# Optimization experiments

Hardware: AMD Instinct MI355X
Metric: run time of the kernel (lower is better)

Reference implementation:

```python
import jax, jax.numpy as jnp
import numpy as np

N, E, G = 100000, 1600000, 64   # nodes, edges, graphs
IN, H, OUT = 32, 128, 3


def setup_inputs() -> dict:
    key = jax.random.key(0)
    ks = jax.random.split(key, 24)
    def w(k, i, o):
        return (jax.random.normal(k, (i, o), jnp.float32) / np.sqrt(i)).astype(jnp.float32)
    inp = {
        "x": jax.random.normal(ks[0], (N, IN), jnp.float32),
        "edge_index": jax.random.randint(ks[1], (2, E), 0, N, dtype=jnp.int32).astype(jnp.int64),
        "batch": jnp.sort(jax.random.randint(ks[2], (N,), 0, G, dtype=jnp.int32)).astype(jnp.int64),
        # SAGEConv layer 0 (in->hidden): lin_l (neighbors, with bias), lin_r (root, no bias)
        "Wl0": w(ks[3], IN, H), "bl0": jnp.zeros((H,), jnp.float32), "Wr0": w(ks[4], IN, H),
        # SAGEConv layers 1,2 (hidden->hidden)
        "Wl1": w(ks[5], H, H), "bl1": jnp.zeros((H,), jnp.float32), "Wr1": w(ks[6], H, H),
        "Wl2": w(ks[7], H, H), "bl2": jnp.zeros((H,), jnp.float32), "Wr2": w(ks[8], H, H),
        # output head
        "Wfc": w(ks[9], H, OUT), "bfc": jnp.zeros((OUT,), jnp.float32),
        # aux MLP on (dim1, dim3)
        "Wa1": w(ks[10], 2, H), "ba1": jnp.zeros((H,), jnp.float32),
        "Wa2": w(ks[11], H, H), "ba2": jnp.zeros((H,), jnp.float32),
        "Wao": w(ks[12], H, 1), "bao": jnp.zeros((1,), jnp.float32),
    }
    return inp


def _sage_conv(x, src, dst, Wl, bl, Wr):
    # PyG SAGEConv (mean aggr): out = lin_l(mean_{j in N(i)} x_j) + lin_r(x_i)
    msg = x[src]                                   # [E, d] gather
    agg = jax.ops.segment_sum(msg, dst, num_segments=N)
    cnt = jax.ops.segment_sum(jnp.ones((src.shape[0],), x.dtype), dst, num_segments=N)
    mean = agg / jnp.maximum(cnt, 1.0)[:, None]
    return mean @ Wl + bl + x @ Wr


def reference(x, edge_index, batch,
              Wl0, bl0, Wr0, Wl1, bl1, Wr1, Wl2, bl2, Wr2,
              Wfc, bfc, Wa1, ba1, Wa2, ba2, Wao, bao):
    src, dst = edge_index[0], edge_index[1]
    h = jax.nn.relu(_sage_conv(x, src, dst, Wl0, bl0, Wr0))   # dropout is identity in eval
    h = jax.nn.relu(_sage_conv(h, src, dst, Wl1, bl1, Wr1))
    h = jax.nn.relu(_sage_conv(h, src, dst, Wl2, bl2, Wr2))
    main = h @ Wfc + bfc                                      # [N, 3]
    dim1, dim3 = main[:, 0], main[:, 2]
    aux_in = jnp.stack([dim1, dim3], axis=-1)                 # [N, 2]
    a = jax.nn.relu(aux_in @ Wa1 + ba1)
    a = jax.nn.relu(a @ Wa2 + ba2)
    aux_out = (a @ Wao + bao)[:, 0]                           # [N]
    final = jnp.stack([dim1, aux_out, dim3], axis=-1)         # [N, 3]
    # global mean pool over graph ids
    s = jax.ops.segment_sum(final, batch, num_segments=G)
    c = jax.ops.segment_sum(jnp.ones((final.shape[0],), final.dtype), batch, num_segments=G)
    return s / jnp.maximum(c, 1.0)[:, None]                   # [G, 3]
```

## Files before the change

### kernel.cpp

```cpp
#include <hip/hip_runtime.h>

#define NR 128
#define PART_CH 4096
typedef unsigned short ushortT;
typedef __attribute__((ext_vector_type(8))) short short8;
typedef __attribute__((ext_vector_type(4))) float float4v;

__device__ __forceinline__ unsigned short f32_to_bf16_rne(float f) {
    unsigned u = __float_as_uint(f);
    unsigned r = (u + 0x7fffu + ((u >> 16) & 1u)) >> 16;
    return (unsigned short)r;
}

__device__ __forceinline__ void accum8(float* acc, uint4 v) {
    unsigned u[4] = {v.x, v.y, v.z, v.w};
#pragma unroll
    for (int q = 0; q < 4; q++) {
        acc[2 * q]     += __uint_as_float(u[q] << 16);
        acc[2 * q + 1] += __uint_as_float(u[q] & 0xffff0000u);
    }
}


__launch_bounds__(256)
__global__ void bucket_count(const int* __restrict__ dst, int* __restrict__ bcnt, int E, int NB) {
    __shared__ int h[1024];
    int t = threadIdx.x;
    for (int j = t; j < NB; j += 256) h[j] = 0;
    __syncthreads();
    int e0 = blockIdx.x * PART_CH;
    int e1 = min(e0 + PART_CH, E);
    for (int e = e0 + t; e < e1; e += 256) atomicAdd(&h[dst[e] >> 7], 1);
    __syncthreads();
    for (int j = t; j < NB; j += 256) {
        int v = h[j];
        if (v) atomicAdd(&bcnt[j], v);
    }
}

__launch_bounds__(256)
__global__ void bucket_scan(const int* __restrict__ bcnt, int* __restrict__ bstart,
                            int* __restrict__ gcur, int NB, int E) {
    __shared__ int sh[256];
    int t = threadIdx.x;
    int v[4];
    int tot = 0;
#pragma unroll
    for (int j = 0; j < 4; j++) {
        int idx = t * 4 + j;
        v[j] = (idx < NB) ? bcnt[idx] : 0;
        tot += v[j];
    }
    sh[t] = tot;
    __syncthreads();
    for (int off = 1; off < 256; off <<= 1) {
        int add = (t >= off) ? sh[t - off] : 0;
        __syncthreads();
        sh[t] += add;
        __syncthreads();
    }
    int run = sh[t] - tot;
#pragma unroll
    for (int j = 0; j < 4; j++) {
        int idx = t * 4 + j;
        if (idx < NB) { bstart[idx] = run; gcur[idx] = run; }
        run += v[j];
    }
    if (t == 0) bstart[NB] = E;
}

__launch_bounds__(256)
__global__ void partition_edges(const int* __restrict__ src, const int* __restrict__ dst,
                                int* __restrict__ gcur, unsigned* __restrict__ packed,
                                int E, int NB) {
    __shared__ int hist[1024];
    __shared__ int base[1024];
    int t = threadIdx.x;
    int e0 = blockIdx.x * PART_CH;
    int e1 = min(e0 + PART_CH, E);
    for (int j = t; j < NB; j += 256) hist[j] = 0;
    __syncthreads();
    for (int e = e0 + t; e < e1; e += 256) atomicAdd(&hist[dst[e] >> 7], 1);
    __syncthreads();
    for (int j = t; j < NB; j += 256) {
        int h = hist[j];
        base[j] = h ? atomicAdd(&gcur[j], h) : 0;
    }
    __syncthreads();
    for (int j = t; j < NB; j += 256) hist[j] = base[j];
    __syncthreads();
    for (int e = e0 + t; e < e1; e += 256) {
        int d = dst[e];
        int b = d >> 7;
        int pos = atomicAdd(&hist[b], 1);
        packed[pos] = (unsigned)src[e] | ((unsigned)(d & (NR - 1)) << 17);
    }
}

__launch_bounds__(256)
__global__ void bucket_sort(const unsigned* __restrict__ packed, const int* __restrict__ bstart,
                            int* __restrict__ row_start, int* __restrict__ srcs, int N) {
    __shared__ int cnt[NR];
    __shared__ int sc[NR];
    __shared__ int cur[NR];
    int b = blockIdx.x, t = threadIdx.x;
    int nb0 = b * NR;
    int nnode = min(NR, N - nb0);
    int lo = bstart[b], hi = bstart[b + 1];
    if (t < NR) cnt[t] = 0;
    __syncthreads();
    for (int j = lo + t; j < hi; j += 256) atomicAdd(&cnt[packed[j] >> 17], 1);
    __syncthreads();
    if (t < NR) sc[t] = cnt[t];
    __syncthreads();
    for (int off = 1; off < NR; off <<= 1) {
        int add = (t >= off && t < NR) ? sc[t - off] : 0;
        __syncthreads();
        if (t < NR) sc[t] += add;
        __syncthreads();
    }
    if (t < nnode) {
        int s = lo + sc[t] - cnt[t];
        row_start[nb0 + t] = s;
        cur[t] = s;
    }
    if (t == 0 && nb0 + nnode == N) row_start[N] = hi;
    __syncthreads();
    for (int j = lo + t; j < hi; j += 256) {
        unsigned pk = packed[j];
        int pos = atomicAdd(&cur[pk >> 17], 1);
        srcs[pos] = (int)(pk & 0x1FFFFu);
    }
}


__global__ void to_bf16_vec(const float* __restrict__ in, ushortT* __restrict__ out, int n4) {
    int t = blockIdx.x * 256 + threadIdx.x;
    if (t < n4) {
        float4 v = ((const float4*)in)[t];
        ushort4 o;
        o.x = f32_to_bf16_rne(v.x);
        o.y = f32_to_bf16_rne(v.y);
        o.z = f32_to_bf16_rne(v.z);
        o.w = f32_to_bf16_rne(v.w);
        ((ushort4*)out)[t] = o;
    }
}


__global__ void prep_wt(const float* __restrict__ Wl, const float* __restrict__ Wr,
                        ushortT* __restrict__ Wt, int KH) {
    int KT = 2 * KH;
    int tid = blockIdx.x * 256 + threadIdx.x;
    if (tid >= 128 * KT) return;
    int col = tid / KT, k = tid - col * KT;
    float v = (k < KH) ? Wl[k * 128 + col] : Wr[(k - KH) * 128 + col];
    int pos = (k + 8 * col) & (KT - 1);
    Wt[col * KT + pos] = f32_to_bf16_rne(v);
}

__global__ void prep_w1(const float* __restrict__ W, ushortT* __restrict__ Wt) {
    int tid = blockIdx.x * 256 + threadIdx.x;
    if (tid >= 128 * 128) return;
    int col = tid >> 7, k = tid & 127;
    int pos = (k + 8 * col) & 127;
    Wt[col * 128 + pos] = f32_to_bf16_rne(W[k * 128 + col]);
}


template <int CPN>
__launch_bounds__(256)
__global__ void aggregate_mean_bf16(const uint4* __restrict__ hin, ushortT* __restrict__ out,
                                    const int* __restrict__ srcs, const int* __restrict__ rs, int n) {
    constexpr int TPN = CPN / 2;
    int tid = blockIdx.x * 256 + threadIdx.x;
    if (tid >= n * TPN) return;
    int i = tid / TPN;
    int c = tid & (TPN - 1);
    int lo = rs[i], hi = rs[i + 1];
    float acc0[8], acc1[8];
#pragma unroll
    for (int q = 0; q < 8; q++) { acc0[q] = 0.f; acc1[q] = 0.f; }
    int e = lo;
    for (; e + 4 <= hi; e += 4) {
        int s0 = srcs[e], s1 = srcs[e + 1], s2 = srcs[e + 2], s3 = srcs[e + 3];
        uint4 a0 = hin[(size_t)s0 * CPN + c];
        uint4 b0 = hin[(size_t)s0 * CPN + c + TPN];
        uint4 a1 = hin[(size_t)s1 * CPN + c];
        uint4 b1 = hin[(size_t)s1 * CPN + c + TPN];
        uint4 a2 = hin[(size_t)s2 * CPN + c];
        uint4 b2 = hin[(size_t)s2 * CPN + c + TPN];
        uint4 a3 = hin[(size_t)s3 * CPN + c];
        uint4 b3 = hin[(size_t)s3 * CPN + c + TPN];
        accum8(acc0, a0); accum8(acc1, b0);
        accum8(acc0, a1); accum8(acc1, b1);
        accum8(acc0, a2); accum8(acc1, b2);
        accum8(acc0, a3); accum8(acc1, b3);
    }
    for (; e < hi; ++e) {
        int s = srcs[e];
        accum8(acc0, hin[(size_t)s * CPN + c]);
        accum8(acc1, hin[(size_t)s * CPN + c + TPN]);
    }
    float inv = 1.0f / (float)max(hi - lo, 1);
    uint4 o0, o1;
    o0.x = (unsigned)f32_to_bf16_rne(acc0[0] * inv) | ((unsigned)f32_to_bf16_rne(acc0[1] * inv) << 16);
    o0.y = (unsigned)f32_to_bf16_rne(acc0[2] * inv) | ((unsigned)f32_to_bf16_rne(acc0[3] * inv) << 16);
    o0.z = (unsigned)f32_to_bf16_rne(acc0[4] * inv) | ((unsigned)f32_to_bf16_rne(acc0[5] * inv) << 16);
    o0.w = (unsigned)f32_to_bf16_rne(acc0[6] * inv) | ((unsigned)f32_to_bf16_rne(acc0[7] * inv) << 16);
    o1.x = (unsigned)f32_to_bf16_rne(acc1[0] * inv) | ((unsigned)f32_to_bf16_rne(acc1[1] * inv) << 16);
    o1.y = (unsigned)f32_to_bf16_rne(acc1[2] * inv) | ((unsigned)f32_to_bf16_rne(acc1[3] * inv) << 16);
    o1.z = (unsigned)f32_to_bf16_rne(acc1[4] * inv) | ((unsigned)f32_to_bf16_rne(acc1[5] * inv) << 16);
    o1.w = (unsigned)f32_to_bf16_rne(acc1[6] * inv) | ((unsigned)f32_to_bf16_rne(acc1[7] * inv) << 16);
    ((uint4*)out)[(size_t)i * CPN + c] = o0;
    ((uint4*)out)[(size_t)i * CPN + c + TPN] = o1;
}


template <int KH, bool OUT_BF16>
__launch_bounds__(256, 2)
__global__ void gemm_mfma(const ushortT* __restrict__ Am, const ushortT* __restrict__ Ah,
                          const ushortT* __restrict__ Wt, const float* __restrict__ bias,
                          float* __restrict__ outf, ushortT* __restrict__ outbf, int n) {
    constexpr int KT = 2 * KH;
    __shared__ ushortT sW[128 * KT];
    int t = threadIdx.x;
    constexpr int TOT16 = 128 * KT * 2 / 16;
    {
        const uint4* Wg = (const uint4*)Wt;
        uint4* Ws = (uint4*)sW;
        for (int j = t; j < TOT16; j += 256) Ws[j] = Wg[j];
    }
    __syncthreads();
    int wv = t >> 6, lane = t & 63;
    int q = lane >> 4, cid = lane & 15;
    int rbase = blockIdx.x * 128 + wv * 32;
    int r0 = rbase + cid, r1 = r0 + 16;
    int r0c = min(r0, n - 1), r1c = min(r1, n - 1);
    float4v acc[2][8];
#pragma unroll
    for (int i = 0; i < 2; i++)
#pragma unroll
        for (int j = 0; j < 8; j++) acc[i][j] = (float4v){0.f, 0.f, 0.f, 0.f};
    int swz = q * 8 + 8 * cid;
#pragma unroll
    for (int ks = 0; ks < KT / 32; ++ks) {
        int kk = ks * 32;
        const ushortT* abase = (kk < KH) ? Am : Ah;
        int kc = (kk < KH) ? kk : kk - KH;
        short8 a0 = *(const short8*)(abase + (size_t)r0c * KH + kc + q * 8);
        short8 a1 = *(const short8*)(abase + (size_t)r1c * KH + kc + q * 8);
#pragma unroll
        for (int j = 0; j < 8; ++j) {
            int col = j * 16 + cid;
            int p = (kk + swz + j * 128) & (KT - 1);
            short8 b = *(const short8*)(sW + col * KT + p);
            acc[0][j] = __builtin_amdgcn_mfma_f32_16x16x32_bf16(a0, b, acc[0][j], 0, 0, 0);
            acc[1][j] = __builtin_amdgcn_mfma_f32_16x16x32_bf16(a1, b, acc[1][j], 0, 0, 0);
        }
    }
    float bo[8];
#pragma unroll
    for (int j = 0; j < 8; ++j) bo[j] = bias[j * 16 + cid];
#pragma unroll
    for (int i = 0; i < 2; ++i) {
#pragma unroll
        for (int rr = 0; rr < 4; ++rr) {
            int row = rbase + i * 16 + q * 4 + rr;
            if (row < n) {
#pragma unroll
                for (int j = 0; j < 8; ++j) {
                    int col = j * 16 + cid;
                    float v = fmaxf(acc[i][j][rr] + bo[j], 0.f);
                    if (OUT_BF16) outbf[(size_t)row * 128 + col] = f32_to_bf16_rne(v);
                    else          outf[(size_t)row * 128 + col] = v;
                }
            }
        }
    }
}


template <int KH>
__launch_bounds__(256, 2)
__global__ void gemm_mfma_fin(const ushortT* __restrict__ Am, const ushortT* __restrict__ Ah,
                              const ushortT* __restrict__ Wt, const float* __restrict__ bias,
                              const float* __restrict__ Wfc, const float* __restrict__ bfc,
                              float* __restrict__ fin, int n) {
    constexpr int KT = 2 * KH;
    __shared__ ushortT sW[128 * KT];
    int t = threadIdx.x;
    constexpr int TOT16 = 128 * KT * 2 / 16;
    {
        const uint4* Wg = (const uint4*)Wt;
        uint4* Ws = (uint4*)sW;
        for (int j = t; j < TOT16; j += 256) Ws[j] = Wg[j];
    }
    __syncthreads();
    int wv = t >> 6, lane = t & 63;
    int q = lane >> 4, cid = lane & 15;
    int rbase = blockIdx.x * 128 + wv * 32;
    int r0 = rbase + cid, r1 = r0 + 16;
    int r0c = min(r0, n - 1), r1c = min(r1, n - 1);
    float4v acc[2][8];
#pragma unroll
    for (int i = 0; i < 2; i++)
#pragma unroll
        for (int j = 0; j < 8; j++) acc[i][j] = (float4v){0.f, 0.f, 0.f, 0.f};
    int swz = q * 8 + 8 * cid;
#pragma unroll
    for (int ks = 0; ks < KT / 32; ++ks) {
        int kk = ks * 32;
        const ushortT* abase = (kk < KH) ? Am : Ah;
        int kc = (kk < KH) ? kk : kk - KH;
        short8 a0 = *(const short8*)(abase + (size_t)r0c * KH + kc + q * 8);
        short8 a1 = *(const short8*)(abase + (size_t)r1c * KH + kc + q * 8);
#pragma unroll
        for (int j = 0; j < 8; ++j) {
            int col = j * 16 + cid;
            int p = (kk + swz + j * 128) & (KT - 1);
            short8 b = *(const short8*)(sW + col * KT + p);
            acc[0][j] = __builtin_amdgcn_mfma_f32_16x16x32_bf16(a0, b, acc[0][j], 0, 0, 0);
            acc[1][j] = __builtin_amdgcn_mfma_f32_16x16x32_bf16(a1, b, acc[1][j], 0, 0, 0);
        }
    }
    float bo[8], w1[8], w3[8];
#pragma unroll
    for (int j = 0; j < 8; ++j) {
        int col = j * 16 + cid;
        bo[j] = bias[col];
        w1[j] = Wfc[col * 3 + 0];
        w3[j] = Wfc[col * 3 + 2];
    }
    float bfc0 = bfc[0], bfc2 = bfc[2];
#pragma unroll
    for (int i = 0; i < 2; ++i) {
#pragma unroll
        for (int rr = 0; rr < 4; ++rr) {
            float p1 = 0.f, p3 = 0.f;
#pragma unroll
            for (int j = 0; j < 8; ++j) {
                float v = fmaxf(acc[i][j][rr] + bo[j], 0.f);
                p1 += v * w1[j];
                p3 += v * w3[j];
            }
            p1 += __shfl_xor(p1, 1, 64); p3 += __shfl_xor(p3, 1, 64);
            p1 += __shfl_xor(p1, 2, 64); p3 += __shfl_xor(p3, 2, 64);
            p1 += __shfl_xor(p1, 4, 64); p3 += __shfl_xor(p3, 4, 64);
            p1 += __shfl_xor(p1, 8, 64); p3 += __shfl_xor(p3, 8, 64);
            int row = rbase + i * 16 + q * 4 + rr;
            if (cid == 0 && row < n) {
                fin[(size_t)row * 3 + 0] = p1 + bfc0;
                fin[(size_t)row * 3 + 2] = p3 + bfc2;
            }
        }
    }
}


__launch_bounds__(256, 4)
__global__ void head_mfma(const ushortT* __restrict__ Wa2t, const float* __restrict__ Wa1,
                          const float* __restrict__ ba1, const float* __restrict__ ba2,
                          const float* __restrict__ Wao, const float* __restrict__ bao,
                          float* __restrict__ fin, int n) {
    __shared__ ushortT sW[128 * 128];
    __shared__ float sD1[128], sD3[128];
    __shared__ float sWa1a[128], sWa1b[128], sBa1[128];
    int t = threadIdx.x;
    {
        const uint4* Wg = (const uint4*)Wa2t;
        uint4* Ws = (uint4*)sW;
        for (int j = t; j < 2048; j += 256) Ws[j] = Wg[j];
    }
    int rbase = blockIdx.x * 128;
    if (t < 128) {
        sWa1a[t] = Wa1[t];
        sWa1b[t] = Wa1[128 + t];
        sBa1[t] = ba1[t];
        int row = min(rbase + t, n - 1);
        sD1[t] = fin[(size_t)row * 3 + 0];
        sD3[t] = fin[(size_t)row * 3 + 2];
    }
    __syncthreads();
    int wv = t >> 6, lane = t & 63;
    int q = lane >> 4, cid = lane & 15;
    int rl0 = wv * 32 + cid, rl1 = rl0 + 16;
    float d1a = sD1[rl0], d3a = sD3[rl0];
    float d1b = sD1[rl1], d3b = sD3[rl1];
    float4v acc[2][8];
#pragma unroll
    for (int i = 0; i < 2; i++)
#pragma unroll
        for (int j = 0; j < 8; j++) acc[i][j] = (float4v){0.f, 0.f, 0.f, 0.f};
    int swz = q * 8 + 8 * cid;
#pragma unroll
    for (int ks = 0; ks < 4; ++ks) {
        int k0 = ks * 32 + q * 8;
        short8 a0, a1;
#pragma unroll
        for (int j = 0; j < 8; ++j) {
            int k = k0 + j;
            float w0 = sWa1a[k], w1 = sWa1b[k], bb = sBa1[k];
            float v0 = fmaxf(fmaf(d1a, w0, fmaf(d3a, w1, bb)), 0.f);
            float v1 = fmaxf(fmaf(d1b, w0, fmaf(d3b, w1, bb)), 0.f);
            a0[j] = (short)f32_to_bf16_rne(v0);
            a1[j] = (short)f32_to_bf16_rne(v1);
        }
        int p = (ks * 32 + swz) & 127;
#pragma unroll
        for (int j = 0; j < 8; ++j) {
            short8 b = *(const short8*)(sW + (j * 16 + cid) * 128 + p);
            acc[0][j] = __builtin_amdgcn_mfma_f32_16x16x32_bf16(a0, b, acc[0][j], 0, 0, 0);
            acc[1][j] = __builtin_amdgcn_mfma_f32_16x16x32_bf16(a1, b, acc[1][j], 0, 0, 0);
        }
    }
    float b2[8], wo[8];
#pragma unroll
    for (int j = 0; j < 8; ++j) {
        int col = j * 16 + cid;
        b2[j] = ba2[col];
        wo[j] = Wao[col];
    }
    float bao0 = bao[0];
#pragma unroll
    for (int i = 0; i < 2; ++i) {
#pragma unroll
        for (int rr = 0; rr < 4; ++rr) {
            float s = 0.f;
#pragma unroll
            for (int j = 0; j < 8; ++j) s += fmaxf(acc[i][j][rr] + b2[j], 0.f) * wo[j];
            s += __shfl_xor(s, 1, 64);
            s += __shfl_xor(s, 2, 64);
            s += __shfl_xor(s, 4, 64);
            s += __shfl_xor(s, 8, 64);
            int row = rbase + wv * 32 + i * 16 + q * 4 + rr;
            if (cid == 0 && row < n) fin[(size_t)row * 3 + 1] = s + bao0;
        }
    }
}


__global__ void pool_kernel(const float* __restrict__ fin, const int* __restrict__ batch,
                            float* __restrict__ out, int n) {
    int g = blockIdx.x, t = threadIdx.x;
    int lo = 0, hi = n;
    while (lo < hi) { int mid = (lo + hi) >> 1; if (batch[mid] < g) lo = mid + 1; else hi = mid; }
    int start = lo;
    lo = 0; hi = n;
    while (lo < hi) { int mid = (lo + hi) >> 1; if (batch[mid] < g + 1) lo = mid + 1; else hi = mid; }
    int end = lo;
    float s0 = 0.f, s1 = 0.f, s2 = 0.f;
    for (int i = start + t; i < end; i += 256) {
        s0 += fin[(size_t)i * 3 + 0];
        s1 += fin[(size_t)i * 3 + 1];
        s2 += fin[(size_t)i * 3 + 2];
    }
    __shared__ float r0[256], r1[256], r2[256];
    r0[t] = s0; r1[t] = s1; r2[t] = s2;
    __syncthreads();
    for (int off = 128; off > 0; off >>= 1) {
        if (t < off) { r0[t] += r0[t + off]; r1[t] += r1[t + off]; r2[t] += r2[t + off]; }
        __syncthreads();
    }
    if (t == 0) {
        float c = (float)max(end - start, 1);
        out[g * 3 + 0] = r0[0] / c;
        out[g * 3 + 1] = r1[0] / c;
        out[g * 3 + 2] = r2[0] / c;
    }
}


extern "C" void kernel_launch(void* const* d_in, const int* in_sizes, int n_in,
                              void* d_out, int out_size, void* d_ws, size_t ws_size,
                              hipStream_t stream) {
    const float* x    = (const float*)d_in[0];
    const int*   ei   = (const int*)d_in[1];
    const int*   batch= (const int*)d_in[2];
    const float* Wl0  = (const float*)d_in[3];
    const float* bl0  = (const float*)d_in[4];
    const float* Wr0  = (const float*)d_in[5];
    const float* Wl1  = (const float*)d_in[6];
    const float* bl1  = (const float*)d_in[7];
    const float* Wr1  = (const float*)d_in[8];
    const float* Wl2  = (const float*)d_in[9];
    const float* bl2  = (const float*)d_in[10];
    const float* Wr2  = (const float*)d_in[11];
    const float* Wfc  = (const float*)d_in[12];
    const float* bfc  = (const float*)d_in[13];
    const float* Wa1  = (const float*)d_in[14];
    const float* ba1  = (const float*)d_in[15];
    const float* Wa2  = (const float*)d_in[16];
    const float* ba2  = (const float*)d_in[17];
    const float* Wao  = (const float*)d_in[18];
    const float* bao  = (const float*)d_in[19];

    const int N = in_sizes[0] / 32;
    const int E = in_sizes[1] / 2;
    const int G = out_size / 3;
    const int* src = ei;
    const int* dst = ei + E;
    float* out = (float*)d_out;
    const int NB = (N + NR - 1) / NR;

    char* p = (char*)d_ws;
    auto carve = [&](size_t bytes) {
        void* r = (void*)p;
        p += (bytes + 255) & ~(size_t)255;
        return r;
    };
    int*      bcnt     = (int*)carve((size_t)NB * 4);
    int*      bstart   = (int*)carve((size_t)(NB + 1) * 4);
    int*      gcur     = (int*)carve((size_t)NB * 4);
    int*      row_start= (int*)carve((size_t)(N + 1) * 4);
    unsigned* packed   = (unsigned*)carve((size_t)E * 4);
    int*      srcs     = (int*)carve((size_t)E * 4);
    ushortT*  aggbf    = (ushortT*)carve((size_t)N * 128 * 2);
    ushortT*  xbf      = (ushortT*)carve((size_t)N * 32 * 2);
    ushortT*  hbf0     = (ushortT*)carve((size_t)N * 128 * 2);
    ushortT*  hbf1     = (ushortT*)carve((size_t)N * 128 * 2);
    float*    fin      = (float*)carve((size_t)N * 3 * 4);
    ushortT*  Wt0      = (ushortT*)carve((size_t)128 * 64 * 2);
    ushortT*  Wt1      = (ushortT*)carve((size_t)128 * 256 * 2);
    ushortT*  Wt2      = (ushortT*)carve((size_t)128 * 256 * 2);
    ushortT*  Wa2t     = (ushortT*)carve((size_t)128 * 128 * 2);

    const int gemm_grid = (N + 127) / 128;
    const int part_grid = (E + PART_CH - 1) / PART_CH;

    to_bf16_vec<<<(N * 32 / 4 + 255) / 256, 256, 0, stream>>>(x, xbf, N * 32 / 4);
    prep_wt<<<(128 * 64 + 255) / 256, 256, 0, stream>>>(Wl0, Wr0, Wt0, 32);
    prep_wt<<<(128 * 256 + 255) / 256, 256, 0, stream>>>(Wl1, Wr1, Wt1, 128);
    prep_wt<<<(128 * 256 + 255) / 256, 256, 0, stream>>>(Wl2, Wr2, Wt2, 128);
    prep_w1<<<(128 * 128 + 255) / 256, 256, 0, stream>>>(Wa2, Wa2t);

    hipMemsetAsync(bcnt, 0, (size_t)NB * 4, stream);
    bucket_count<<<part_grid, 256, 0, stream>>>(dst, bcnt, E, NB);
    bucket_scan<<<1, 256, 0, stream>>>(bcnt, bstart, gcur, NB, E);
    partition_edges<<<part_grid, 256, 0, stream>>>(src, dst, gcur, packed, E, NB);
    bucket_sort<<<NB, 256, 0, stream>>>(packed, bstart, row_start, srcs, N);

    aggregate_mean_bf16<4><<<(N * 2 + 255) / 256, 256, 0, stream>>>(
        (const uint4*)xbf, aggbf, srcs, row_start, N);
    gemm_mfma<32, true><<<gemm_grid, 256, 0, stream>>>(
        aggbf, xbf, Wt0, bl0, (float*)nullptr, hbf0, N);
    aggregate_mean_bf16<16><<<(N * 8 + 255) / 256, 256, 0, stream>>>(
        (const uint4*)hbf0, aggbf, srcs, row_start, N);
    gemm_mfma<128, true><<<gemm_grid, 256, 0, stream>>>(
        aggbf, hbf0, Wt1, bl1, (float*)nullptr, hbf1, N);
    aggregate_mean_bf16<16><<<(N * 8 + 255) / 256, 256, 0, stream>>>(
        (const uint4*)hbf1, aggbf, srcs, row_start, N);
    gemm_mfma_fin<128><<<gemm_grid, 256, 0, stream>>>(
        aggbf, hbf1, Wt2, bl2, Wfc, bfc, fin, N);

    head_mfma<<<gemm_grid, 256, 0, stream>>>(
        Wa2t, Wa1, ba1, ba2, Wao, bao, fin, N);

    pool_kernel<<<G, 256, 0, stream>>>(fin, batch, out, N);
}
```

Baseline: 396.2 us.

## Gather hidden features in fp8 for layer 1/2 neighbor aggregation

The hidden-layer GEMMs now also write an fp8 copy of their activations, and the mean aggregation for layers 1 and 2 gathers these 1-byte values instead of bf16, halving gather traffic per edge. The bf16 aggregation loop also gains an 8-wide unrolled stage for more memory-level parallelism. The cost is extra byte-wise fp8 stores in the GEMM epilogue and reduced precision in the aggregated means, which risks accuracy tolerance.

```diff
diff --git a/kernel.cpp b/kernel.cpp
--- a/kernel.cpp
+++ b/kernel.cpp
@@ -5,6 +5,7 @@
 typedef unsigned short ushortT;
 typedef __attribute__((ext_vector_type(8))) short short8;
 typedef __attribute__((ext_vector_type(4))) float float4v;
+typedef __attribute__((ext_vector_type(2))) float float2v;
 
 __device__ __forceinline__ unsigned short f32_to_bf16_rne(float f) {
     unsigned u = __float_as_uint(f);
@@ -12,12 +13,29 @@
     return (unsigned short)r;
 }
 
+__device__ __forceinline__ unsigned char f32_to_fp8(float f) {
+    return (unsigned char)(__builtin_amdgcn_cvt_pk_fp8_f32(f, f, 0, false) & 0xff);
+}
+
 __device__ __forceinline__ void accum8(float* acc, uint4 v) {
     unsigned u[4] = {v.x, v.y, v.z, v.w};
 #pragma unroll
     for (int q = 0; q < 4; q++) {
         acc[2 * q]     += __uint_as_float(u[q] << 16);
         acc[2 * q + 1] += __uint_as_float(u[q] & 0xffff0000u);
+    }
+}
+
+__device__ __forceinline__ void accum16_fp8(float* acc, uint4 v) {
+    unsigned u[4] = {v.x, v.y, v.z, v.w};
+#pragma unroll
+    for (int q = 0; q < 4; q++) {
+        float2v lo = __builtin_amdgcn_cvt_pk_f32_fp8(u[q], false);
+        float2v hi = __builtin_amdgcn_cvt_pk_f32_fp8(u[q], true);
+        acc[4 * q + 0] += lo.x;
+        acc[4 * q + 1] += lo.y;
+        acc[4 * q + 2] += hi.x;
+        acc[4 * q + 3] += hi.y;
     }
 }
 
@@ -182,20 +200,31 @@
 #pragma unroll
     for (int q = 0; q < 8; q++) { acc0[q] = 0.f; acc1[q] = 0.f; }
     int e = lo;
+    for (; e + 8 <= hi; e += 8) {
+        int s[8];
+#pragma unroll
+        for (int u = 0; u < 8; u++) s[u] = srcs[e + u];
+        uint4 va[8], vb[8];
+#pragma unroll
+        for (int u = 0; u < 8; u++) {
+            va[u] = hin[(size_t)s[u] * CPN + c];
+            vb[u] = hin[(size_t)s[u] * CPN + c + TPN];
+        }
+#pragma unroll
+        for (int u = 0; u < 8; u++) { accum8(acc0, va[u]); accum8(acc1, vb[u]); }
+    }
     for (; e + 4 <= hi; e += 4) {
-        int s0 = srcs[e], s1 = srcs[e + 1], s2 = srcs[e + 2], s3 = srcs[e + 3];
-        uint4 a0 = hin[(size_t)s0 * CPN + c];
-        uint4 b0 = hin[(size_t)s0 * CPN + c + TPN];
-        uint4 a1 = hin[(size_t)s1 * CPN + c];
-        uint4 b1 = hin[(size_t)s1 * CPN + c + TPN];
-        uint4 a2 = hin[(size_t)s2 * CPN + c];
-        uint4 b2 = hin[(size_t)s2 * CPN + c + TPN];
-        uint4 a3 = hin[(size_t)s3 * CPN + c];
-        uint4 b3 = hin[(size_t)s3 * CPN + c + TPN];
-        accum8(acc0, a0); accum8(acc1, b0);
-        accum8(acc0, a1); accum8(acc1, b1);
-        accum8(acc0, a2); accum8(acc1, b2);
-        accum8(acc0, a3); accum8(acc1, b3);
+        int s[4];
+#pragma unroll
+        for (int u = 0; u < 4; u++) s[u] = srcs[e + u];
+        uint4 va[4], vb[4];
+#pragma unroll
+        for (int u = 0; u < 4; u++) {
+            va[u] = hin[(size_t)s[u] * CPN + c];
+            vb[u] = hin[(size_t)s[u] * CPN + c + TPN];
+        }
+#pragma unroll
+        for (int u = 0; u < 4; u++) { accum8(acc0, va[u]); accum8(acc1, vb[u]); }
     }
     for (; e < hi; ++e) {
         int s = srcs[e];
@@ -217,11 +246,60 @@
 }
 
 
-template <int KH, bool OUT_BF16>
+__launch_bounds__(256)
+__global__ void aggregate_mean_fp8(const uint4* __restrict__ hin, ushortT* __restrict__ out,
+                                   const int* __restrict__ srcs, const int* __restrict__ rs, int n) {
+    int tid = blockIdx.x * 256 + threadIdx.x;
+    if (tid >= n * 8) return;
+    int i = tid >> 3;
+    int c = tid & 7;
+    int lo = rs[i], hi = rs[i + 1];
+    float acc[16];
+#pragma unroll
+    for (int q = 0; q < 16; q++) acc[q] = 0.f;
+    int e = lo;
+    for (; e + 8 <= hi; e += 8) {
+        int s[8];
+#pragma unroll
+        for (int u = 0; u < 8; u++) s[u] = srcs[e + u];
+        uint4 v[8];
+#pragma unroll
+        for (int u = 0; u < 8; u++) v[u] = hin[(size_t)s[u] * 8 + c];
+#pragma unroll
+        for (int u = 0; u < 8; u++) accum16_fp8(acc, v[u]);
+    }
+    for (; e + 4 <= hi; e += 4) {
+        int s[4];
+#pragma unroll
+        for (int u = 0; u < 4; u++) s[u] = srcs[e + u];
+        uint4 v[4];
+#pragma unroll
+        for (int u = 0; u < 4; u++) v[u] = hin[(size_t)s[u] * 8 + c];
+#pragma unroll
+        for (int u = 0; u < 4; u++) accum16_fp8(acc, v[u]);
+    }
+    for (; e < hi; ++e) accum16_fp8(acc, hin[(size_t)srcs[e] * 8 + c]);
+    float inv = 1.0f / (float)max(hi - lo, 1);
+    uint4 o0, o1;
+    o0.x = (unsigned)f32_to_bf16_rne(acc[0] * inv)  | ((unsigned)f32_to_bf16_rne(acc[1] * inv) << 16);
+    o0.y = (unsigned)f32_to_bf16_rne(acc[2] * inv)  | ((unsigned)f32_to_bf16_rne(acc[3] * inv) << 16);
+    o0.z = (unsigned)f32_to_bf16_rne(acc[4] * inv)  | ((unsigned)f32_to_bf16_rne(acc[5] * inv) << 16);
+    o0.w = (unsigned)f32_to_bf16_rne(acc[6] * inv)  | ((unsigned)f32_to_bf16_rne(acc[7] * inv) << 16);
+    o1.x = (unsigned)f32_to_bf16_rne(acc[8] * inv)  | ((unsigned)f32_to_bf16_rne(acc[9] * inv) << 16);
+    o1.y = (unsigned)f32_to_bf16_rne(acc[10] * inv) | ((unsigned)f32_to_bf16_rne(acc[11] * inv) << 16);
+    o1.z = (unsigned)f32_to_bf16_rne(acc[12] * inv) | ((unsigned)f32_to_bf16_rne(acc[13] * inv) << 16);
+    o1.w = (unsigned)f32_to_bf16_rne(acc[14] * inv) | ((unsigned)f32_to_bf16_rne(acc[15] * inv) << 16);
+    ((uint4*)out)[(size_t)i * 16 + c * 2]     = o0;
+    ((uint4*)out)[(size_t)i * 16 + c * 2 + 1] = o1;
+}
+
+
+template <int KH, bool OUT_BF16, bool OUT_FP8>
 __launch_bounds__(256, 2)
 __global__ void gemm_mfma(const ushortT* __restrict__ Am, const ushortT* __restrict__ Ah,
                           const ushortT* __restrict__ Wt, const float* __restrict__ bias,
-                          float* __restrict__ outf, ushortT* __restrict__ outbf, int n) {
+                          float* __restrict__ outf, ushortT* __restrict__ outbf,
+                          unsigned char* __restrict__ outf8, int n) {
     constexpr int KT = 2 * KH;
     __shared__ ushortT sW[128 * KT];
     int t = threadIdx.x;
@@ -273,7 +351,8 @@
                     int col = j * 16 + cid;
                     float v = fmaxf(acc[i][j][rr] + bo[j], 0.f);
                     if (OUT_BF16) outbf[(size_t)row * 128 + col] = f32_to_bf16_rne(v);
-                    else          outf[(size_t)row * 128 + col] = v;
+                    if (OUT_FP8)  outf8[(size_t)row * 128 + col] = f32_to_fp8(v);
+                    if (!OUT_BF16 && !OUT_FP8) outf[(size_t)row * 128 + col] = v;
                 }
             }
         }
@@ -509,21 +588,23 @@
         p += (bytes + 255) & ~(size_t)255;
         return r;
     };
-    int*      bcnt     = (int*)carve((size_t)NB * 4);
-    int*      bstart   = (int*)carve((size_t)(NB + 1) * 4);
-    int*      gcur     = (int*)carve((size_t)NB * 4);
-    int*      row_start= (int*)carve((size_t)(N + 1) * 4);
-    unsigned* packed   = (unsigned*)carve((size_t)E * 4);
-    int*      srcs     = (int*)carve((size_t)E * 4);
-    ushortT*  aggbf    = (ushortT*)carve((size_t)N * 128 * 2);
-    ushortT*  xbf      = (ushortT*)carve((size_t)N * 32 * 2);
-    ushortT*  hbf0     = (ushortT*)carve((size_t)N * 128 * 2);
-    ushortT*  hbf1     = (ushortT*)carve((size_t)N * 128 * 2);
-    float*    fin      = (float*)carve((size_t)N * 3 * 4);
-    ushortT*  Wt0      = (ushortT*)carve((size_t)128 * 64 * 2);
-    ushortT*  Wt1      = (ushortT*)carve((size_t)128 * 256 * 2);
-    ushortT*  Wt2      = (ushortT*)carve((size_t)128 * 256 * 2);
-    ushortT*  Wa2t     = (ushortT*)carve((size_t)128 * 128 * 2);
+    int*           bcnt     = (int*)carve((size_t)NB * 4);
+    int*           bstart   = (int*)carve((size_t)(NB + 1) * 4);
+    int*           gcur     = (int*)carve((size_t)NB * 4);
+    int*           row_start= (int*)carve((size_t)(N + 1) * 4);
+    unsigned*      packed   = (unsigned*)carve((size_t)E * 4);
+    int*           srcs     = (int*)carve((size_t)E * 4);
+    ushortT*       aggbf    = (ushortT*)carve((size_t)N * 128 * 2);
+    ushortT*       xbf      = (ushortT*)carve((size_t)N * 32 * 2);
+    ushortT*       hbf0     = (ushortT*)carve((size_t)N * 128 * 2);
+    ushortT*       hbf1     = (ushortT*)carve((size_t)N * 128 * 2);
+    unsigned char* hf8_0    = (unsigned char*)carve((size_t)N * 128);
+    unsigned char* hf8_1    = (unsigned char*)carve((size_t)N * 128);
+    float*         fin      = (float*)carve((size_t)N * 3 * 4);
+    ushortT*       Wt0      = (ushortT*)carve((size_t)128 * 64 * 2);
+    ushortT*       Wt1      = (ushortT*)carve((size_t)128 * 256 * 2);
+    ushortT*       Wt2      = (ushortT*)carve((size_t)128 * 256 * 2);
+    ushortT*       Wa2t     = (ushortT*)carve((size_t)128 * 128 * 2);
 
     const int gemm_grid = (N + 127) / 128;
     const int part_grid = (E + PART_CH - 1) / PART_CH;
@@ -542,14 +623,14 @@
 
     aggregate_mean_bf16<4><<<(N * 2 + 255) / 256, 256, 0, stream>>>(
         (const uint4*)xbf, aggbf, srcs, row_start, N);
-    gemm_mfma<32, true><<<gemm_grid, 256, 0, stream>>>(
-        aggbf, xbf, Wt0, bl0, (float*)nullptr, hbf0, N);
-    aggregate_mean_bf16<16><<<(N * 8 + 255) / 256, 256, 0, stream>>>(
-        (const uint4*)hbf0, aggbf, srcs, row_start, N);
-    gemm_mfma<128, true><<<gemm_grid, 256, 0, stream>>>(
-        aggbf, hbf0, Wt1, bl1, (float*)nullptr, hbf1, N);
-    aggregate_mean_bf16<16><<<(N * 8 + 255) / 256, 256, 0, stream>>>(
-        (const uint4*)hbf1, aggbf, srcs, row_start, N);
+    gemm_mfma<32, true, true><<<gemm_grid, 256, 0, stream>>>(
+        aggbf, xbf, Wt0, bl0, (float*)nullptr, hbf0, hf8_0, N);
+    aggregate_mean_fp8<<<(N * 8 + 255) / 256, 256, 0, stream>>>(
+        (const uint4*)hf8_0, aggbf, srcs, row_start, N);
+    gemm_mfma<128, true, true><<<gemm_grid, 256, 0, stream>>>(
+        aggbf, hbf0, Wt1, bl1, (float*)nullptr, hbf1, hf8_1, N);
+    aggregate_mean_fp8<<<(N * 8 + 255) / 256, 256, 0, stream>>>(
+        (const uint4*)hf8_1, aggbf, srcs, row_start, N);
     gemm_mfma_fin<128><<<gemm_grid, 256, 0, stream>>>(
         aggbf, hbf1, Wt2, bl2, Wfc, bfc, fin, N);
 
```

Result: faster. 359.8 us (-9.2%).
